# Optimization experiments

Measured on AMD Instinct MI355X. Metric: run time of the kernel, lower is better.

Reference implementation:

```python
import jax, jax.numpy as jnp
import numpy as np

B, T, M, C, H = 32, 128, 1290, 512, 8
NUM_BLOCKS = 4
MLP_LAYERS = 2
TOPK = 8


def _ln(x, g, b):
    mu = jnp.mean(x, -1, keepdims=True)
    var = jnp.mean((x - mu) ** 2, -1, keepdims=True)
    return (x - mu) / jnp.sqrt(var + 1e-5) * g + b


def setup_inputs() -> dict:
    key = jax.random.key(0)
    ks = jax.random.split(key, 12)

    def w(k, shape, s=0.02):
        return jax.random.normal(k, shape, jnp.float32) * s

    return {
        "ipts": jax.random.normal(ks[0], (B, T, C), jnp.float32),
        "memory": jax.random.normal(ks[1], (B, M, C), jnp.float32),
        "Wq": w(ks[2], (C, C)), "bq": jnp.zeros(C, jnp.float32),
        "Wk": w(ks[3], (C, C)), "bk": jnp.zeros(C, jnp.float32),
        "Wv": w(ks[4], (C, C)), "bv": jnp.zeros(C, jnp.float32),
        "Wm": w(ks[5], (C, C)), "bm": jnp.zeros(C, jnp.float32),  # shared attention_mlp layer
        "g1": jnp.ones(C, jnp.float32), "b1": jnp.zeros(C, jnp.float32),
        "g2": jnp.ones(C, jnp.float32), "b2": jnp.zeros(C, jnp.float32),
        "Wp": w(ks[6], (C, C)), "bp": jnp.zeros(C, jnp.float32),
        "rep_w": jax.random.normal(ks[7], (C,), jnp.float32),
        "Wig": w(ks[8], (C, 2 * C)), "big": jnp.zeros(2 * C, jnp.float32),
        "Wmg": w(ks[9], (C, 2 * C)), "bmg": jnp.zeros(2 * C, jnp.float32),
        "forget_bias": jnp.float32(1.0),
        "input_bias": jnp.float32(0.0),
    }


def reference(ipts, memory, Wq, bq, Wk, bk, Wv, bv, Wm, bm, g1, b1, g2, b2,
              Wp, bp, rep_w, Wig, big, Wmg, bmg, forget_bias, input_bias):
    Dh = C // H
    scale = 1.0 / np.sqrt(Dh)

    def heads(x):  # [B,L,C] -> [B,H,L,Dh]
        return x.reshape(x.shape[0], x.shape[1], H, Dh).transpose(0, 2, 1, 3)

    def mha(inp, mem, use_topk):
        # query from mem, key/value from inp (matches multi_head_attention(ipts, memory))
        q, k, v = heads(mem @ Wq + bq), heads(inp @ Wk + bk), heads(inp @ Wv + bv)
        att = jax.nn.softmax(jnp.einsum('bhqd,bhkd->bhqk', q, k) * scale, axis=-1)
        if use_topk:
            _, idx = jax.lax.top_k(att, TOPK)  # [B,H,Q,TOPK]
            mask = jnp.zeros_like(att)
            for i in range(TOPK):  # small fixed loop; avoids [.,.,.,K,L] blowup
                mask = mask + jax.nn.one_hot(idx[..., i], att.shape[-1], dtype=att.dtype)
            att = att * mask
        o = jnp.einsum('bhqk,bhkd->bhqd', att, v)
        return o.transpose(0, 2, 1, 3).reshape(o.shape[0], o.shape[2], C)

    inp = ipts @ Wp + bp  # input_projector, [B,T,C]
    mem = memory
    for _ in range(NUM_BLOCKS):
        mem = _ln(mem + mha(inp, mem, True), g1, b1)
        h = mem
        for _ in range(MLP_LAYERS):  # shared weights (ModuleList([lin]*L))
            h = jax.nn.relu(h @ Wm + bm)
        mem = _ln(mem + h, g2, b2)

    # gates (gate_style='unit')
    gi = jnp.mean(jax.nn.relu(rep_w * inp), axis=1) @ Wig + big  # [B,2C]
    gm = jnp.tanh(memory) @ Wmg + bmg                            # [B,M,2C]
    gates = gm + gi[:, None, :]
    ig = jax.nn.sigmoid(gates[..., :C] + input_bias)
    fg = jax.nn.sigmoid(gates[..., C:] + forget_bias)
    next_memory = ig * jnp.tanh(mem) + fg * memory

    # hx: query from inp, key/value from next_memory, no topk
    hx = mha(next_memory, inp, False)  # [B,T,C]
    return (next_memory, hx)
```

## Files before the change

kernel.cpp:

```cpp
#include <hip/hip_runtime.h>
#include <stdint.h>

typedef uint16_t u16;
typedef uint32_t u32;

#define DEVI __device__ __forceinline__

DEVI float b2f(u16 u) { return __uint_as_float(((u32)u) << 16); }
DEVI float blo(u32 u) { return __uint_as_float(u << 16); }
DEVI float bhi(u32 u) { return __uint_as_float(u & 0xffff0000u); }
DEVI u16 f2b(float f) {
  u32 x = __float_as_uint(f);
  return (u16)((x + 0x7fffu + ((x >> 16) & 1u)) >> 16);
}
DEVI u32 pack2(float a, float b) { return (u32)f2b(a) | ((u32)f2b(b) << 16); }
DEVI float sigm(float x) { return 1.f / (1.f + __expf(-x)); }
DEVI float ftanh(float x) { return 1.f - 2.f / (1.f + __expf(2.f * x)); }

typedef __bf16 bf16x8 __attribute__((ext_vector_type(8)));
typedef float f32x4 __attribute__((ext_vector_type(4)));

#define MFMA16(a, b, c) __builtin_amdgcn_mfma_f32_16x16x32_bf16(a, b, c, 0, 0, 0)

DEVI void gll16(const void* g, void* l) {
  __builtin_amdgcn_global_load_lds((const __attribute__((address_space(1))) void*)g,
                                   (__attribute__((address_space(3))) void*)l, 16, 0, 0);
}

DEVI u32 fmono(float s) {
  u32 x = __float_as_uint(s);
  return x ^ (((u32)((int)x >> 31)) | 0x80000000u);
}

DEVI void ced(u32& a, u32& b) {
  u32 hi = max(a, b), lo = min(a, b);
  a = hi; b = lo;
}
DEVI void sort8_desc(u32* v) {
  ced(v[0], v[1]); ced(v[2], v[3]); ced(v[4], v[5]); ced(v[6], v[7]);
  ced(v[0], v[2]); ced(v[1], v[3]); ced(v[4], v[6]); ced(v[5], v[7]);
  ced(v[1], v[2]); ced(v[5], v[6]);
  ced(v[0], v[4]); ced(v[1], v[5]); ced(v[2], v[6]); ced(v[3], v[7]);
  ced(v[2], v[4]); ced(v[3], v[5]);
  ced(v[1], v[2]); ced(v[3], v[4]); ced(v[5], v[6]);
}
DEVI void bitonic8_desc(u32* v) {
  ced(v[0], v[4]); ced(v[1], v[5]); ced(v[2], v[6]); ced(v[3], v[7]);
  ced(v[0], v[2]); ced(v[1], v[3]); ced(v[4], v[6]); ced(v[5], v[7]);
  ced(v[0], v[1]); ced(v[2], v[3]); ced(v[4], v[5]); ced(v[6], v[7]);
}
DEVI void merge_top8(u32* a, const u32* b) {
#pragma unroll
  for (int j = 0; j < 8; ++j) a[j] = max(a[j], b[7 - j]);
  bitonic8_desc(a);
}

__global__ void detect_kernel(const u16* __restrict__ x, int* __restrict__ flag) {
  if (threadIdx.x == 0 && blockIdx.x == 0) {
    int f = 0;
    for (int i = 0; i < 64; ++i) {
      u16 u = x[2 * i];
      int e = (u >> 7) & 0xFF;
      if (e > 131) f = 1;
    }
    *flag = f;
  }
}

struct CvtArgs {
  const void* src[23];
  int aoff[23];
  int n[23];
  int total;
};

__global__ __launch_bounds__(256) void convert_fused(CvtArgs a, u16* __restrict__ arena,
                                                     const int* __restrict__ flag) {
  int e4 = (blockIdx.x * 256 + threadIdx.x) * 4;
  if (e4 >= a.total) return;
  const char* sp = (const char*)a.src[0];
  int rel = e4, cnt = a.n[0];
#pragma unroll
  for (int j = 1; j < 23; ++j)
    if (e4 >= a.aoff[j]) { sp = (const char*)a.src[j]; rel = e4 - a.aoff[j]; cnt = a.n[j]; }
  const bool f32 = (*flag != 0);
  if (rel + 3 < cnt) {
    if (f32) {
      float4 v = *(const float4*)(sp + (size_t)rel * 4);
      uint2 o;
      o.x = pack2(v.x, v.y);
      o.y = pack2(v.z, v.w);
      *(uint2*)(arena + e4) = o;
    } else {
      *(uint2*)(arena + e4) = *(const uint2*)(sp + (size_t)rel * 2);
    }
  } else {
#pragma unroll
    for (int k = 0; k < 4; ++k) {
      u16 o = 0;
      if (rel + k < cnt)
        o = f32 ? f2b(((const float*)sp)[rel + k]) : ((const u16*)sp)[rel + k];
      arena[e4 + k] = o;
    }
  }
}

__global__ void biascat_kernel(const u16* __restrict__ bq, const u16* __restrict__ bk,
                               const u16* __restrict__ bv, u16* __restrict__ bqkv,
                               u16* __restrict__ bkv) {
  int t = threadIdx.x;
  bqkv[t] = bq[t];
  bqkv[512 + t] = bk[t];
  bqkv[1024 + t] = bv[t];
  bkv[t] = bk[t];
  bkv[512 + t] = bv[t];
}

template <int ACT>
__global__ __launch_bounds__(256, 4) void gemm_bt(
    const u16* __restrict__ A, const u16* __restrict__ Bt,
    const u16* __restrict__ bias, u16* __restrict__ Co, int Mtot, int Ntot, int nby) {
  __shared__ __align__(16) u16 smem[128 * 136];
  u16* const aB0 = smem;
  u16* const aB1 = smem + 4096;
  u16* const bB0 = smem + 8192;
  u16* const bB1 = smem + 12288;
  const int tid = threadIdx.x;
  const int lane = tid & 63;
  const int w = tid >> 6;
  const int quad = lane >> 4;
  const int l15 = lane & 15;

  const int nwg = gridDim.x;
  const int orig = blockIdx.x;
  const int xcd = orig & 7, sq = orig >> 3;
  const int qd = nwg >> 3, rm = nwg & 7;
  const int wg = (xcd < rm ? xcd * (qd + 1) : rm * (qd + 1) + (xcd - rm) * qd) + sq;
  const int m0 = (wg / nby) * 128;
  const int n0 = (wg % nby) * 128;

  const int wm = (w & 1) << 6;
  const int wn = (w >> 1) << 6;

  f32x4 acc[4][4] = {};

  const u16* ga[2];
  const u16* gb[2];
#pragma unroll
  for (int q = 0; q < 2; ++q) {
    int j = q * 256 + tid;
    int r = j >> 2, s = j & 3;
    int c = (s ^ ((r >> 1) & 3)) * 8;
    int ra = m0 + r;
    if (ra >= Mtot) ra = Mtot - 1;
    ga[q] = A + (size_t)ra * 512 + c;
    gb[q] = Bt + (size_t)(n0 + r) * 512 + c;
  }

  auto stage = [&](int p, int ko) {
    u16* ab = p ? aB1 : aB0;
    u16* bb = p ? bB1 : bB0;
#pragma unroll
    for (int q = 0; q < 2; ++q) {
      int j = q * 256 + tid;
      gll16(ga[q] + ko * 32, ab + j * 8);
      gll16(gb[q] + ko * 32, bb + j * 8);
    }
  };

  stage(0, 0);
  __syncthreads();
  int cur = 0;
  for (int ko = 0; ko < 16; ++ko) {
    if (ko < 15) stage(cur ^ 1, ko + 1);
    u16* ab = cur ? aB1 : aB0;
    u16* bb = cur ? bB1 : bB0;
    bf16x8 af[4], bfr[4];
#pragma unroll
    for (int i = 0; i < 4; ++i) {
      int r = wm + i * 16 + l15;
      af[i] = *(const bf16x8*)(ab + (((r << 2) | (quad ^ ((r >> 1) & 3)))) * 8);
      int rn = wn + i * 16 + l15;
      bfr[i] = *(const bf16x8*)(bb + (((rn << 2) | (quad ^ ((rn >> 1) & 3)))) * 8);
    }
#pragma unroll
    for (int i = 0; i < 4; ++i)
#pragma unroll
      for (int jn = 0; jn < 4; ++jn)
        acc[i][jn] = MFMA16(af[i], bfr[jn], acc[i][jn]);
    __syncthreads();
    cur ^= 1;
  }

  u16* st = smem;
  const int cl = l15;
  const int rg = quad;
#pragma unroll
  for (int jn = 0; jn < 4; ++jn) {
    int coll = wn + jn * 16 + cl;
    float bv = b2f(bias[n0 + coll]);
#pragma unroll
    for (int i = 0; i < 4; ++i) {
      int rowb = wm + i * 16 + rg * 4;
#pragma unroll
      for (int rr = 0; rr < 4; ++rr) {
        float vv = acc[i][jn][rr] + bv;
        if (ACT) vv = fmaxf(vv, 0.f);
        st[(rowb + rr) * 136 + coll] = f2b(vv);
      }
    }
  }
  __syncthreads();
#pragma unroll
  for (int t = 0; t < 8; ++t) {
    int idx = (t * 256 + tid) * 8;
    int r = idx >> 7;
    int c = idx & 127;
    int row = m0 + r;
    if (row < Mtot) {
      uint4 v = *(const uint4*)(st + r * 136 + c);
      *(uint4*)(Co + (size_t)row * Ntot + n0 + c) = v;
    }
  }
}

__global__ __launch_bounds__(256, 4) void gemm_gates(
    const u16* __restrict__ A, const u16* __restrict__ WmgTp,
    const u16* __restrict__ bmg, const u16* __restrict__ gi,
    const u16* __restrict__ memfin, const u16* __restrict__ mem_in,
    const u16* __restrict__ ibp, const u16* __restrict__ fbp,
    u16* __restrict__ nmbf, void* __restrict__ outp, const int* __restrict__ flag,
    int Mtot) {
  __shared__ __align__(16) u16 smem[128 * 136];
  u16* const aB0 = smem;
  u16* const aB1 = smem + 4096;
  u16* const bB0 = smem + 8192;
  u16* const bB1 = smem + 12288;
  const int tid = threadIdx.x;
  const int lane = tid & 63;
  const int w = tid >> 6;
  const int quad = lane >> 4;
  const int l15 = lane & 15;

  const int nwg = gridDim.x;
  const int orig = blockIdx.x;
  const int xcd = orig & 7, sq = orig >> 3;
  const int qd = nwg >> 3, rm = nwg & 7;
  const int wg = (xcd < rm ? xcd * (qd + 1) : rm * (qd + 1) + (xcd - rm) * qd) + sq;
  const int m0 = (wg >> 3) * 128;
  const int n0h = (wg & 7) * 64;

  const int wm = (w & 1) << 6;
  const int wn = (w >> 1) << 6;

  f32x4 acc[4][4] = {};

  const u16* ga[2];
  const u16* gb[2];
#pragma unroll
  for (int q = 0; q < 2; ++q) {
    int j = q * 256 + tid;
    int r = j >> 2, s = j & 3;
    int c = (s ^ ((r >> 1) & 3)) * 8;
    int ra = m0 + r;
    if (ra >= Mtot) ra = Mtot - 1;
    ga[q] = A + (size_t)ra * 512 + c;
    int br = (r < 64) ? (n0h + r) : (512 + n0h + r - 64);
    gb[q] = WmgTp + (size_t)br * 512 + c;
  }

  auto stage = [&](int p, int ko) {
    u16* ab = p ? aB1 : aB0;
    u16* bb = p ? bB1 : bB0;
#pragma unroll
    for (int q = 0; q < 2; ++q) {
      int j = q * 256 + tid;
      gll16(ga[q] + ko * 32, ab + j * 8);
      gll16(gb[q] + ko * 32, bb + j * 8);
    }
  };

  stage(0, 0);
  __syncthreads();
  int cur = 0;
  for (int ko = 0; ko < 16; ++ko) {
    if (ko < 15) stage(cur ^ 1, ko + 1);
    u16* ab = cur ? aB1 : aB0;
    u16* bb = cur ? bB1 : bB0;
    bf16x8 af[4], bfr[4];
#pragma unroll
    for (int i = 0; i < 4; ++i) {
      int r = wm + i * 16 + l15;
      af[i] = *(const bf16x8*)(ab + (((r << 2) | (quad ^ ((r >> 1) & 3)))) * 8);
      int rn = wn + i * 16 + l15;
      bfr[i] = *(const bf16x8*)(bb + (((rn << 2) | (quad ^ ((rn >> 1) & 3)))) * 8);
    }
#pragma unroll
    for (int i = 0; i < 4; ++i)
#pragma unroll
      for (int jn = 0; jn < 4; ++jn)
        acc[i][jn] = MFMA16(af[i], bfr[jn], acc[i][jn]);
    __syncthreads();
    cur ^= 1;
  }

  u16* st = smem;
#pragma unroll
  for (int jn = 0; jn < 4; ++jn) {
    int coll = wn + jn * 16 + l15;
    int bcol = (coll < 64) ? (n0h + coll) : (512 + n0h + coll - 64);
    float bv = b2f(bmg[bcol]);
#pragma unroll
    for (int i = 0; i < 4; ++i) {
      int rowb = wm + i * 16 + quad * 4;
#pragma unroll
      for (int rr = 0; rr < 4; ++rr)
        st[(rowb + rr) * 136 + coll] = f2b(acc[i][jn][rr] + bv);
    }
  }
  __syncthreads();

  const float ib = b2f(ibp[0]);
  const float fb = b2f(fbp[0]);
  const bool of32 = (*flag != 0);
#pragma unroll
  for (int t = 0; t < 4; ++t) {
    int chunk = t * 256 + tid;
    int rl = chunk >> 3;
    int c8 = (chunk & 7) * 8;
    int row = m0 + rl;
    if (row >= Mtot) continue;
    int b = row / 1290;
    size_t gidx = (size_t)row * 512 + n0h + c8;
    uint4 uig = *(const uint4*)(st + rl * 136 + c8);
    uint4 ufg = *(const uint4*)(st + rl * 136 + 64 + c8);
    uint4 ugi = *(const uint4*)(gi + b * 1024 + n0h + c8);
    uint4 ugf = *(const uint4*)(gi + b * 1024 + 512 + n0h + c8);
    uint4 umf = *(const uint4*)(memfin + gidx);
    uint4 umi = *(const uint4*)(mem_in + gidx);
    const u32* pig = (const u32*)&uig;
    const u32* pfg = (const u32*)&ufg;
    const u32* pgi = (const u32*)&ugi;
    const u32* pgf = (const u32*)&ugf;
    const u32* pmf = (const u32*)&umf;
    const u32* pmi = (const u32*)&umi;
    float v[8];
#pragma unroll
    for (int k = 0; k < 4; ++k) {
      float ig0 = sigm(blo(pig[k]) + blo(pgi[k]) + ib);
      float ig1 = sigm(bhi(pig[k]) + bhi(pgi[k]) + ib);
      float fg0 = sigm(blo(pfg[k]) + blo(pgf[k]) + fb);
      float fg1 = sigm(bhi(pfg[k]) + bhi(pgf[k]) + fb);
      v[2 * k] = ig0 * ftanh(blo(pmf[k])) + fg0 * blo(pmi[k]);
      v[2 * k + 1] = ig1 * ftanh(bhi(pmf[k])) + fg1 * bhi(pmi[k]);
    }
    uint4 o;
    u32* po = (u32*)&o;
#pragma unroll
    for (int k = 0; k < 4; ++k) po[k] = pack2(v[2 * k], v[2 * k + 1]);
    *(uint4*)(nmbf + gidx) = o;
    if (of32) {
      float4 f0, f1;
      f0.x = v[0]; f0.y = v[1]; f0.z = v[2]; f0.w = v[3];
      f1.x = v[4]; f1.y = v[5]; f1.z = v[6]; f1.w = v[7];
      *(float4*)((float*)outp + gidx) = f0;
      *(float4*)((float*)outp + gidx + 4) = f1;
    } else {
      *(uint4*)((u16*)outp + gidx) = o;
    }
  }
}

__global__ __launch_bounds__(256) void transpose_kernel(const u16* __restrict__ in,
                                                        u16* __restrict__ outb, int K, int N) {
  __shared__ u16 tile[32][33];
  const int tx = threadIdx.x & 31, ty = threadIdx.x >> 5;
  const int bx = blockIdx.x * 32;
  const int by = blockIdx.y * 32;
#pragma unroll
  for (int i = 0; i < 32; i += 8) tile[ty + i][tx] = in[(size_t)(by + ty + i) * N + bx + tx];
  __syncthreads();
#pragma unroll
  for (int i = 0; i < 32; i += 8) outb[(size_t)(bx + ty + i) * K + by + tx] = tile[tx][ty + i];
}

__global__ void tanhmem_kernel(const u16* __restrict__ mi, u16* __restrict__ th, int n8) {
  int i = blockIdx.x * 256 + threadIdx.x;
  if (i >= n8) return;
  uint4 u = ((const uint4*)mi)[i];
  uint4 t;
  t.x = pack2(ftanh(blo(u.x)), ftanh(bhi(u.x)));
  t.y = pack2(ftanh(blo(u.y)), ftanh(bhi(u.y)));
  t.z = pack2(ftanh(blo(u.z)), ftanh(bhi(u.z)));
  t.w = pack2(ftanh(blo(u.w)), ftanh(bhi(u.w)));
  ((uint4*)th)[i] = t;
}

__global__ void redmean_kernel(const u16* __restrict__ inp, const u16* __restrict__ repw,
                               u16* __restrict__ outb) {
  const int b = blockIdx.x;
  const int c = blockIdx.y * 256 + threadIdx.x;
  const float rw = b2f(repw[c]);
  float s = 0.f;
  for (int t = 0; t < 128; ++t)
    s += fmaxf(rw * b2f(inp[(size_t)(b * 128 + t) * 512 + c]), 0.f);
  outb[b * 512 + c] = f2b(s * (1.f / 128.f));
}

__global__ __launch_bounds__(256) void ln_kernel(const u16* __restrict__ src,
                                                 const u16* __restrict__ addb,
                                                 u16* __restrict__ dst,
                                                 const u16* __restrict__ g,
                                                 const u16* __restrict__ bb) {
  const int row = blockIdx.x * 4 + (threadIdx.x >> 6);
  const int lane = threadIdx.x & 63;
  const u16* srow = src + (size_t)row * 512;
  const u16* arow = addb + (size_t)row * 512;
  float x[8];
  float s = 0.f;
#pragma unroll
  for (int i = 0; i < 8; ++i) {
    int c = lane + i * 64;
    x[i] = b2f(srow[c]) + b2f(arow[c]);
    s += x[i];
  }
#pragma unroll
  for (int off = 32; off > 0; off >>= 1) s += __shfl_xor(s, off, 64);
  const float mu = s * (1.f / 512.f);
  float v = 0.f;
#pragma unroll
  for (int i = 0; i < 8; ++i) {
    float d = x[i] - mu;
    v = fmaf(d, d, v);
  }
#pragma unroll
  for (int off = 32; off > 0; off >>= 1) v += __shfl_xor(v, off, 64);
  const float rstd = rsqrtf(v * (1.f / 512.f) + 1e-5f);
  u16* orow = dst + (size_t)row * 512;
#pragma unroll
  for (int i = 0; i < 8; ++i) {
    int c = lane + i * 64;
    orow[c] = f2b(fmaf((x[i] - mu) * rstd, b2f(g[c]), b2f(bb[c])));
  }
}

__global__ __launch_bounds__(256, 3) void attn1_mfma(const u16* __restrict__ q,
                                                     const u16* __restrict__ kb,
                                                     const u16* __restrict__ vb,
                                                     u16* __restrict__ o, int ldkv) {
  __shared__ __align__(16) u16 Pl[128 * 136];
  __shared__ __align__(16) u16 VT[64 * 136];
  __shared__ float lbuf[128];
  u16* Kl = Pl;

  const int tid = threadIdx.x;
  const int lane = tid & 63;
  const int w = tid >> 6;
  const int quad = lane >> 4;
  const int l15 = lane & 15;
  const int qb = blockIdx.x;
  const int bh = blockIdx.y;
  const int b = bh >> 3, h = bh & 7;

#pragma unroll
  for (int qq = 0; qq < 4; ++qq) {
    int j = qq * 256 + tid;
    int r = j >> 3, s = j & 7;
    gll16(kb + (size_t)(b * 128 + r) * ldkv + h * 64 + (s ^ (r & 7)) * 8, Kl + j * 8);
  }
#pragma unroll
  for (int p = 0; p < 4; ++p) {
    int key = (tid & 63) + 64 * (p & 1);
    int dc = w + 4 * (p >> 1);
    uint4 u = *(const uint4*)(vb + (size_t)(b * 128 + key) * ldkv + h * 64 + dc * 8);
    u16 tmp[8];
    *(uint4*)tmp = u;
#pragma unroll
    for (int jj = 0; jj < 8; ++jj) VT[(dc * 8 + jj) * 136 + key] = tmp[jj];
  }

  bf16x8 bq[2][2];
  {
    int ra = min(qb * 128 + w * 32 + l15, 1289);
    int rb_ = min(qb * 128 + w * 32 + 16 + l15, 1289);
    const u16* qa = q + (size_t)(b * 1290 + ra) * 512 + h * 64 + quad * 8;
    const u16* qc = q + (size_t)(b * 1290 + rb_) * 512 + h * 64 + quad * 8;
    bq[0][0] = *(const bf16x8*)(qa);
    bq[0][1] = *(const bf16x8*)(qa + 32);
    bq[1][0] = *(const bf16x8*)(qc);
    bq[1][1] = *(const bf16x8*)(qc + 32);
  }
  __syncthreads();

  f32x4 sa[2][8] = {};
#pragma unroll
  for (int ks = 0; ks < 2; ++ks) {
#pragma unroll
    for (int jn = 0; jn < 8; ++jn) {
      int n = jn * 16 + l15;
      int cch = ks * 4 + quad;
      bf16x8 ak = *(const bf16x8*)(Kl + (n * 8 + (cch ^ (n & 7))) * 8);
      sa[0][jn] = MFMA16(ak, bq[0][ks], sa[0][jn]);
      sa[1][jn] = MFMA16(ak, bq[1][ks], sa[1][jn]);
    }
  }
  __syncthreads();

  const u32 ibase = 127u - (u32)(quad * 4);
#pragma unroll
  for (int i = 0; i < 2; ++i) {
    const int qi = w * 32 + i * 16 + l15;
    u32 g[4][8];
#pragma unroll
    for (int jn = 0; jn < 8; ++jn)
#pragma unroll
      for (int rr = 0; rr < 4; ++rr) {
        float s = sa[i][jn][rr] * 0.125f;
        sa[i][jn][rr] = s;
        g[jn >> 1][(jn & 1) * 4 + rr] =
            (fmono(s) & 0xFFFFFF80u) | (ibase - (u32)(jn * 16 + rr));
      }
    sort8_desc(g[0]); sort8_desc(g[1]); sort8_desc(g[2]); sort8_desc(g[3]);
    merge_top8(g[0], g[1]);
    merge_top8(g[2], g[3]);
    merge_top8(g[0], g[2]);
    u32* tv = g[0];
#pragma unroll
    for (int off = 16; off < 64; off <<= 1) {
      u32 pv[8];
#pragma unroll
      for (int j = 0; j < 8; ++j) pv[j] = (u32)__shfl_xor((int)tv[7 - j], off, 64);
#pragma unroll
      for (int j = 0; j < 8; ++j) tv[j] = max(tv[j], pv[j]);
      bitonic8_desc(tv);
    }
    const u32 t8 = tv[7];
    u32 mb = tv[0] & 0xFFFFFF80u;
    u32 xm = (mb & 0x80000000u) ? (mb ^ 0x80000000u) : ~mb;
    const float mx = __uint_as_float(xm);
    float lsum = 0.f;
#pragma unroll
    for (int jn = 0; jn < 8; ++jn) {
      u16 pr[4];
#pragma unroll
      for (int rr = 0; rr < 4; ++rr) {
        float s = sa[i][jn][rr];
        float e = __expf(s - mx);
        lsum += e;
        u32 kk = (fmono(s) & 0xFFFFFF80u) | (ibase - (u32)(jn * 16 + rr));
        pr[rr] = (kk >= t8) ? f2b(e) : (u16)0;
      }
      uint2 st;
      st.x = (u32)pr[0] | ((u32)pr[1] << 16);
      st.y = (u32)pr[2] | ((u32)pr[3] << 16);
      *(uint2*)(Pl + qi * 136 + jn * 16 + quad * 4) = st;
    }
    lsum += __shfl_xor(lsum, 16, 64);
    lsum += __shfl_xor(lsum, 32, 64);
    if (quad == 0) lbuf[qi] = 1.f / lsum;
  }
  __syncthreads();

  f32x4 oa[2][4] = {};
#pragma unroll
  for (int kc = 0; kc < 4; ++kc) {
    bf16x8 ap[2];
#pragma unroll
    for (int i = 0; i < 2; ++i)
      ap[i] = *(const bf16x8*)(Pl + (w * 32 + i * 16 + l15) * 136 + kc * 32 + quad * 8);
#pragma unroll
    for (int jd = 0; jd < 4; ++jd) {
      bf16x8 bv_ = *(const bf16x8*)(VT + (jd * 16 + l15) * 136 + kc * 32 + quad * 8);
      oa[0][jd] = MFMA16(ap[0], bv_, oa[0][jd]);
      oa[1][jd] = MFMA16(ap[1], bv_, oa[1][jd]);
    }
  }

#pragma unroll
  for (int i = 0; i < 2; ++i) {
    int rowl = w * 32 + i * 16 + quad * 4;
#pragma unroll
    for (int rr = 0; rr < 4; ++rr) {
      int qg = qb * 128 + rowl + rr;
      if (qg < 1290) {
        float il = lbuf[rowl + rr];
        u16* orow = o + (size_t)(b * 1290 + qg) * 512 + h * 64;
#pragma unroll
        for (int jd = 0; jd < 4; ++jd) orow[jd * 16 + l15] = f2b(oa[i][jd][rr] * il);
      }
    }
  }
}

__global__ __launch_bounds__(256, 2) void attn2_mfma(const u16* __restrict__ q2,
                                                     const u16* __restrict__ k2,
                                                     const u16* __restrict__ v2,
                                                     float* __restrict__ pacc,
                                                     float* __restrict__ pml,
                                                     int ldq, int ldkv) {
  __shared__ __align__(16) u16 Kl[64 * 64];
  __shared__ __align__(16) u16 VT[64 * 72];
  __shared__ __align__(16) u16 Pl[4 * 32 * 72];
  const int tid = threadIdx.x;
  const int lane = tid & 63;
  const int w = tid >> 6;
  const int quad = lane >> 4;
  const int l15 = lane & 15;
  const int bh = blockIdx.x;
  const int b = bh >> 3, h = bh & 7;
  const int part = blockIdx.y;
  const int kstart = (part * 1290) >> 2;
  const int kend = ((part + 1) * 1290) >> 2;

  bf16x8 aq[2][2];
  {
    int r0 = b * 128 + w * 32 + l15;
    const u16* qa = q2 + (size_t)r0 * ldq + h * 64 + quad * 8;
    aq[0][0] = *(const bf16x8*)(qa);
    aq[0][1] = *(const bf16x8*)(qa + 32);
    aq[1][0] = *(const bf16x8*)(qa + (size_t)16 * ldq);
    aq[1][1] = *(const bf16x8*)(qa + (size_t)16 * ldq + 32);
  }

  f32x4 oa[2][4] = {};
  float m_[2][4], l_[2][4];
#pragma unroll
  for (int i = 0; i < 2; ++i)
#pragma unroll
    for (int r = 0; r < 4; ++r) { m_[i][r] = -1e30f; l_[i][r] = 0.f; }

  const int nk = kend - kstart;
  for (int kt = 0; kt < nk; kt += 64) {
    __syncthreads();
#pragma unroll
    for (int qq = 0; qq < 2; ++qq) {
      int j = qq * 256 + tid;
      int r = j >> 3, s = j & 7;
      int kg = kstart + kt + r;
      if (kg >= kend) kg = kend - 1;
      gll16(k2 + (size_t)(b * 1290 + kg) * ldkv + h * 64 + (s ^ (r & 7)) * 8, Kl + j * 8);
    }
    {
      int r = tid & 63;
      int kg = kstart + kt + r;
      if (kg >= kend) kg = kend - 1;
      const u16* vrow = v2 + (size_t)(b * 1290 + kg) * ldkv + h * 64;
#pragma unroll
      for (int p = 0; p < 2; ++p) {
        int dc = (tid >> 6) + p * 4;
        uint4 u = *(const uint4*)(vrow + dc * 8);
        u16 tmp[8];
        *(uint4*)tmp = u;
#pragma unroll
        for (int jj = 0; jj < 8; ++jj) VT[(dc * 8 + jj) * 72 + r] = tmp[jj];
      }
    }
    __syncthreads();

    f32x4 sa[2][4] = {};
#pragma unroll
    for (int ks = 0; ks < 2; ++ks) {
#pragma unroll
      for (int jn = 0; jn < 4; ++jn) {
        int n = jn * 16 + l15;
        int cch = ks * 4 + quad;
        bf16x8 bk = *(const bf16x8*)(Kl + (n * 8 + (cch ^ (n & 7))) * 8);
        sa[0][jn] = MFMA16(aq[0][ks], bk, sa[0][jn]);
        sa[1][jn] = MFMA16(aq[1][ks], bk, sa[1][jn]);
      }
    }

    u16* pw = Pl + w * (32 * 72);
#pragma unroll
    for (int i = 0; i < 2; ++i) {
      float rmax[4] = {-1e30f, -1e30f, -1e30f, -1e30f};
#pragma unroll
      for (int jn = 0; jn < 4; ++jn) {
        int kg = kstart + kt + jn * 16 + l15;
        bool val = kg < kend;
#pragma unroll
        for (int r = 0; r < 4; ++r) {
          float s = sa[i][jn][r] * 0.125f;
          s = val ? s : -1e30f;
          sa[i][jn][r] = s;
          rmax[r] = fmaxf(rmax[r], s);
        }
      }
#pragma unroll
      for (int off = 1; off < 16; off <<= 1)
#pragma unroll
        for (int r = 0; r < 4; ++r) rmax[r] = fmaxf(rmax[r], __shfl_xor(rmax[r], off, 64));
      float alpha[4];
#pragma unroll
      for (int r = 0; r < 4; ++r) {
        float mn = fmaxf(m_[i][r], rmax[r]);
        alpha[r] = __expf(m_[i][r] - mn);
        m_[i][r] = mn;
      }
      float lsum[4] = {0.f, 0.f, 0.f, 0.f};
#pragma unroll
      for (int jn = 0; jn < 4; ++jn)
#pragma unroll
        for (int r = 0; r < 4; ++r) {
          float p = __expf(sa[i][jn][r] - m_[i][r]);
          sa[i][jn][r] = p;
          lsum[r] += p;
        }
#pragma unroll
      for (int off = 1; off < 16; off <<= 1)
#pragma unroll
        for (int r = 0; r < 4; ++r) lsum[r] += __shfl_xor(lsum[r], off, 64);
#pragma unroll
      for (int r = 0; r < 4; ++r) l_[i][r] = l_[i][r] * alpha[r] + lsum[r];
#pragma unroll
      for (int jd = 0; jd < 4; ++jd)
#pragma unroll
        for (int r = 0; r < 4; ++r) oa[i][jd][r] *= alpha[r];
#pragma unroll
      for (int jn = 0; jn < 4; ++jn) {
        int col = jn * 16 + l15;
#pragma unroll
        for (int r = 0; r < 4; ++r)
          pw[(i * 16 + quad * 4 + r) * 72 + col] = f2b(sa[i][jn][r]);
      }
    }

#pragma unroll
    for (int ks = 0; ks < 2; ++ks) {
      bf16x8 ap[2];
#pragma unroll
      for (int i = 0; i < 2; ++i)
        ap[i] = *(const bf16x8*)(pw + (i * 16 + l15) * 72 + ks * 32 + quad * 8);
#pragma unroll
      for (int jd = 0; jd < 4; ++jd) {
        bf16x8 bv_ = *(const bf16x8*)(VT + (jd * 16 + l15) * 72 + ks * 32 + quad * 8);
        oa[0][jd] = MFMA16(ap[0], bv_, oa[0][jd]);
        oa[1][jd] = MFMA16(ap[1], bv_, oa[1][jd]);
      }
    }
  }

  float* pa = pacc + (size_t)(part * 256 + bh) * 128 * 64;
#pragma unroll
  for (int i = 0; i < 2; ++i) {
    int row = w * 32 + i * 16 + quad * 4;
#pragma unroll
    for (int r = 0; r < 4; ++r)
#pragma unroll
      for (int jd = 0; jd < 4; ++jd)
        pa[(size_t)(row + r) * 64 + jd * 16 + l15] = oa[i][jd][r];
    if (l15 == 0) {
#pragma unroll
      for (int r = 0; r < 4; ++r) {
        size_t pi = (size_t)(part * 256 + bh) * 128 + row + r;
        pml[pi * 2 + 0] = m_[i][r];
        pml[pi * 2 + 1] = l_[i][r];
      }
    }
  }
}

__global__ __launch_bounds__(64) void attn2_merge(const float* __restrict__ pacc,
                                                  const float* __restrict__ pml,
                                                  void* __restrict__ outp,
                                                  const int* __restrict__ flag) {
  const int qi = blockIdx.x;
  const int bh = qi >> 7, t = qi & 127;
  const int b = bh >> 3, h = bh & 7;
  const int lane = threadIdx.x;
  float mv[4], lv[4];
  float m0 = -1e30f;
#pragma unroll
  for (int i = 0; i < 4; ++i) {
    size_t pi = (size_t)(i * 256 + bh) * 128 + t;
    mv[i] = pml[pi * 2];
    lv[i] = pml[pi * 2 + 1];
    m0 = fmaxf(m0, mv[i]);
  }
  float L = 0.f, accd = 0.f;
#pragma unroll
  for (int i = 0; i < 4; ++i) {
    size_t pi = (size_t)(i * 256 + bh) * 128 + t;
    float e = __expf(mv[i] - m0);
    L += lv[i] * e;
    accd += pacc[pi * 64 + lane] * e;
  }
  float v = accd / L;
  size_t off = (size_t)41280 * 512 + ((size_t)(b * 128 + t) * 512 + h * 64 + lane);
  if (*flag) ((float*)outp)[off] = v; else ((u16*)outp)[off] = f2b(v);
}

extern "C" void kernel_launch(void* const* d_in, const int* in_sizes, int n_in,
                              void* d_out, int out_size, void* d_ws, size_t ws_size,
                              hipStream_t stream) {
  (void)out_size; (void)ws_size;
  char* ws = (char*)d_ws;
  size_t off = 0;
  auto alloc = [&](size_t bytes) {
    char* p = ws + off;
    off += (bytes + 255) & ~(size_t)255;
    return (void*)p;
  };

  int* flag = (int*)alloc(256);

  size_t aoffs[32];
  size_t total = 0;
  for (int i = 0; i < n_in; ++i) {
    aoffs[i] = total;
    total += ((size_t)in_sizes[i] + 127) & ~(size_t)127;
  }
  u16* arena = (u16*)alloc(total * 2);

  const u16* c_ipts = arena + aoffs[0];
  const u16* c_mem  = arena + aoffs[1];
  const u16* c_Wq = arena + aoffs[2];  const u16* c_bq = arena + aoffs[3];
  const u16* c_Wk = arena + aoffs[4];  const u16* c_bk = arena + aoffs[5];
  const u16* c_Wv = arena + aoffs[6];  const u16* c_bv = arena + aoffs[7];
  const u16* c_Wm = arena + aoffs[8];  const u16* c_bm = arena + aoffs[9];
  const u16* c_g1 = arena + aoffs[10]; const u16* c_b1 = arena + aoffs[11];
  const u16* c_g2 = arena + aoffs[12]; const u16* c_b2 = arena + aoffs[13];
  const u16* c_Wp = arena + aoffs[14]; const u16* c_bp = arena + aoffs[15];
  const u16* c_repw = arena + aoffs[16];
  const u16* c_Wig = arena + aoffs[17]; const u16* c_big = arena + aoffs[18];
  const u16* c_Wmg = arena + aoffs[19]; const u16* c_bmg = arena + aoffs[20];
  const u16* c_fb = arena + aoffs[21];
  const u16* c_ib = arena + aoffs[22];

  u16* WqkvT = (u16*)alloc((size_t)1536 * 512 * 2);
  u16* WmT = (u16*)alloc(512 * 512 * 2);
  u16* WpT = (u16*)alloc(512 * 512 * 2);
  u16* WigT = (u16*)alloc(512 * 1024 * 2);
  u16* WmgT = (u16*)alloc(512 * 1024 * 2);
  u16* bqkv = (u16*)alloc(1536 * 2);
  u16* bkv = (u16*)alloc(1024 * 2);
  u16* inp = (u16*)alloc((size_t)4096 * 512 * 2);
  u16* qkvbuf = (u16*)alloc((size_t)4096 * 1536 * 2);
  u16* rmean = (u16*)alloc(32 * 512 * 2);
  u16* gi = (u16*)alloc(32 * 1024 * 2);
  u16* membf = (u16*)alloc((size_t)41280 * 512 * 2);
  u16* qbuf = (u16*)alloc((size_t)41280 * 512 * 2);
  u16* obuf = (u16*)alloc((size_t)41280 * 512 * 2);
  u16* gmbuf = (u16*)alloc((size_t)41280 * 512 * 2);
  u16* nmbf = (u16*)alloc((size_t)41280 * 512 * 2);
  (void)gmbuf;
  u16* kvbuf = obuf;
  float* pacc = (float*)(void*)qbuf;
  float* pml = (float*)((char*)(void*)qbuf + (size_t)4 * 32768 * 64 * 4);

  detect_kernel<<<1, 64, 0, stream>>>((const u16*)d_in[0], flag);
  {
    CvtArgs ca;
    for (int i = 0; i < 23; ++i) {
      int ii = (i < n_in) ? i : (n_in - 1);
      ca.src[i] = d_in[ii];
      ca.aoff[i] = (int)aoffs[ii];
      ca.n[i] = in_sizes[ii];
    }
    ca.total = (int)total;
    convert_fused<<<(unsigned)((total / 4 + 255) / 256), 256, 0, stream>>>(ca, arena, flag);
  }
  biascat_kernel<<<1, 512, 0, stream>>>(c_bq, c_bk, c_bv, bqkv, bkv);

  transpose_kernel<<<dim3(16, 16), 256, 0, stream>>>(c_Wq, WqkvT, 512, 512);
  transpose_kernel<<<dim3(16, 16), 256, 0, stream>>>(c_Wk, WqkvT + (size_t)512 * 512, 512, 512);
  transpose_kernel<<<dim3(16, 16), 256, 0, stream>>>(c_Wv, WqkvT + (size_t)1024 * 512, 512, 512);
  transpose_kernel<<<dim3(16, 16), 256, 0, stream>>>(c_Wm, WmT, 512, 512);
  transpose_kernel<<<dim3(16, 16), 256, 0, stream>>>(c_Wp, WpT, 512, 512);
  transpose_kernel<<<dim3(32, 16), 256, 0, stream>>>(c_Wig, WigT, 512, 1024);
  transpose_kernel<<<dim3(32, 16), 256, 0, stream>>>(c_Wmg, WmgT, 512, 1024);

  gemm_bt<0><<<dim3(32 * 4), 256, 0, stream>>>(c_ipts, WpT, c_bp, inp, 4096, 512, 4);
  gemm_bt<0><<<dim3(32 * 12), 256, 0, stream>>>(inp, WqkvT, bqkv, qkvbuf, 4096, 1536, 12);

  redmean_kernel<<<dim3(32, 2), 256, 0, stream>>>(inp, c_repw, rmean);
  gemm_bt<0><<<dim3(1 * 8), 256, 0, stream>>>(rmean, WigT, c_big, gi, 32, 1024, 8);

  const u16* memsrc = c_mem;
  for (int it = 0; it < 4; ++it) {
    gemm_bt<0><<<dim3(323 * 4), 256, 0, stream>>>(memsrc, WqkvT, c_bq, qbuf, 41280, 512, 4);
    attn1_mfma<<<dim3(11, 256), 256, 0, stream>>>(qbuf, qkvbuf + 512, qkvbuf + 1024, obuf, 1536);
    ln_kernel<<<dim3(10320), 256, 0, stream>>>(memsrc, obuf, membf, c_g1, c_b1);
    gemm_bt<1><<<dim3(323 * 4), 256, 0, stream>>>(membf, WmT, c_bm, qbuf, 41280, 512, 4);
    gemm_bt<1><<<dim3(323 * 4), 256, 0, stream>>>(qbuf, WmT, c_bm, obuf, 41280, 512, 4);
    ln_kernel<<<dim3(10320), 256, 0, stream>>>(membf, obuf, membf, c_g2, c_b2);
    memsrc = membf;
  }

  tanhmem_kernel<<<dim3(2641920 / 256), 256, 0, stream>>>(c_mem, qbuf, 2641920);
  gemm_gates<<<dim3(323 * 8), 256, 0, stream>>>(qbuf, WmgT, c_bmg, gi, membf, c_mem,
                                                c_ib, c_fb, nmbf, d_out, flag, 41280);

  gemm_bt<0><<<dim3(323 * 8), 256, 0, stream>>>(nmbf, WqkvT + (size_t)512 * 512, bkv,
                                                kvbuf, 41280, 1024, 8);
  attn2_mfma<<<dim3(256, 4), 256, 0, stream>>>(qkvbuf, kvbuf, kvbuf + 512, pacc, pml,
                                               1536, 1024);
  attn2_merge<<<dim3(32768), 64, 0, stream>>>(pacc, pml, d_out, flag);
}
```

Baseline: 1.188 ms.

## Fuse two shared-weight MLP layers and second layernorm into one kernel

Replaces the two MLP GEMM launches and the following layernorm with a single kernel that keeps a 64-row tile of the first layer's activations in LDS, runs the second GEMM from LDS, and applies residual plus layernorm in registers before writing back in place. This removes the global-memory round trips of two full-size intermediate activations and two launches per block iteration. In exchange it uses large LDS per block (lower occupancy), loads weight fragments directly from global/L2 without LDS staging, and has fewer blocks than the original tiled GEMMs.

```diff
diff --git a/kernel.cpp b/kernel.cpp
--- a/kernel.cpp
+++ b/kernel.cpp
@@ -221,6 +221,150 @@
       uint4 v = *(const uint4*)(st + r * 136 + c);
       *(uint4*)(Co + (size_t)row * Ntot + n0 + c) = v;
     }
+  }
+}
+
+__global__ __launch_bounds__(256, 2) void gemm_mlp_ln(
+    u16* __restrict__ mem, const u16* __restrict__ WmT, const u16* __restrict__ bm,
+    const u16* __restrict__ g2, const u16* __restrict__ b2) {
+  __shared__ __align__(16) u16 h1[64 * 512];
+  __shared__ __align__(16) u16 ast[2][64 * 32];
+  __shared__ float red[4][64][2];
+  const int tid = threadIdx.x;
+  const int lane = tid & 63;
+  const int w = tid >> 6;
+  const int quad = lane >> 4;
+  const int l15 = lane & 15;
+  const int m0 = blockIdx.x * 64;
+  const int nw = w * 128;
+
+  const int sr = tid >> 2, ss = tid & 3;
+  const u16* ga = mem + (size_t)(m0 + sr) * 512 + ((ss ^ ((sr >> 1) & 3)) * 8);
+
+  f32x4 acc[4][8] = {};
+
+  gll16(ga, &ast[0][0] + tid * 8);
+  __syncthreads();
+  for (int ko = 0; ko < 16; ++ko) {
+    if (ko < 15) gll16(ga + (ko + 1) * 32, &ast[(ko + 1) & 1][0] + tid * 8);
+    const u16* ab = &ast[ko & 1][0];
+    bf16x8 af[4];
+#pragma unroll
+    for (int i = 0; i < 4; ++i) {
+      int r = i * 16 + l15;
+      af[i] = *(const bf16x8*)(ab + (((r << 2) | (quad ^ ((r >> 1) & 3)))) * 8);
+    }
+#pragma unroll
+    for (int j = 0; j < 8; ++j) {
+      int col = nw + j * 16 + l15;
+      bf16x8 bfr = *(const bf16x8*)(WmT + (size_t)col * 512 + ko * 32 + quad * 8);
+#pragma unroll
+      for (int i = 0; i < 4; ++i) acc[i][j] = MFMA16(af[i], bfr, acc[i][j]);
+    }
+    __syncthreads();
+  }
+
+#pragma unroll
+  for (int j = 0; j < 8; ++j) {
+    int col = nw + j * 16 + l15;
+    float bv = b2f(bm[col]);
+    int chunk = col >> 3, cin = col & 7;
+#pragma unroll
+    for (int i = 0; i < 4; ++i)
+#pragma unroll
+      for (int rr = 0; rr < 4; ++rr) {
+        int row = i * 16 + quad * 4 + rr;
+        h1[row * 512 + ((chunk ^ (row & 7)) << 3) + cin] =
+            f2b(fmaxf(acc[i][j][rr] + bv, 0.f));
+      }
+  }
+  __syncthreads();
+
+#pragma unroll
+  for (int i = 0; i < 4; ++i)
+#pragma unroll
+    for (int j = 0; j < 8; ++j) acc[i][j] = (f32x4){0.f, 0.f, 0.f, 0.f};
+  for (int ko = 0; ko < 16; ++ko) {
+    bf16x8 af[4];
+#pragma unroll
+    for (int i = 0; i < 4; ++i) {
+      int r = i * 16 + l15;
+      af[i] = *(const bf16x8*)(h1 + r * 512 + ((((ko << 2) + quad) ^ (r & 7)) << 3));
+    }
+#pragma unroll
+    for (int j = 0; j < 8; ++j) {
+      int col = nw + j * 16 + l15;
+      bf16x8 bfr = *(const bf16x8*)(WmT + (size_t)col * 512 + ko * 32 + quad * 8);
+#pragma unroll
+      for (int i = 0; i < 4; ++i) acc[i][j] = MFMA16(af[i], bfr, acc[i][j]);
+    }
+  }
+
+  float ps[4][4], pq[4][4];
+#pragma unroll
+  for (int i = 0; i < 4; ++i)
+#pragma unroll
+    for (int rr = 0; rr < 4; ++rr) { ps[i][rr] = 0.f; pq[i][rr] = 0.f; }
+#pragma unroll
+  for (int j = 0; j < 8; ++j) {
+    int col = nw + j * 16 + l15;
+    float bv = b2f(bm[col]);
+#pragma unroll
+    for (int i = 0; i < 4; ++i)
+#pragma unroll
+      for (int rr = 0; rr < 4; ++rr) {
+        int row = i * 16 + quad * 4 + rr;
+        float h2 = fmaxf(acc[i][j][rr] + bv, 0.f);
+        float x = b2f(f2b(h2)) + b2f(mem[(size_t)(m0 + row) * 512 + col]);
+        acc[i][j][rr] = x;
+        ps[i][rr] += x;
+        pq[i][rr] = fmaf(x, x, pq[i][rr]);
+      }
+  }
+#pragma unroll
+  for (int off = 1; off < 16; off <<= 1)
+#pragma unroll
+    for (int i = 0; i < 4; ++i)
+#pragma unroll
+      for (int rr = 0; rr < 4; ++rr) {
+        ps[i][rr] += __shfl_xor(ps[i][rr], off, 64);
+        pq[i][rr] += __shfl_xor(pq[i][rr], off, 64);
+      }
+  if (l15 == 0) {
+#pragma unroll
+    for (int i = 0; i < 4; ++i)
+#pragma unroll
+      for (int rr = 0; rr < 4; ++rr) {
+        int row = i * 16 + quad * 4 + rr;
+        red[w][row][0] = ps[i][rr];
+        red[w][row][1] = pq[i][rr];
+      }
+  }
+  __syncthreads();
+
+#pragma unroll
+  for (int i = 0; i < 4; ++i)
+#pragma unroll
+    for (int rr = 0; rr < 4; ++rr) {
+      int row = i * 16 + quad * 4 + rr;
+      float s = red[0][row][0] + red[1][row][0] + red[2][row][0] + red[3][row][0];
+      float q = red[0][row][1] + red[1][row][1] + red[2][row][1] + red[3][row][1];
+      float mu = s * (1.f / 512.f);
+      float var = fmaxf(q * (1.f / 512.f) - mu * mu, 0.f);
+      float rstd = rsqrtf(var + 1e-5f);
+#pragma unroll
+      for (int j = 0; j < 8; ++j) {
+        int col = nw + j * 16 + l15;
+        h1[row * 512 + col] =
+            f2b(fmaf((acc[i][j][rr] - mu) * rstd, b2f(g2[col]), b2f(b2[col])));
+      }
+    }
+  __syncthreads();
+#pragma unroll
+  for (int t = 0; t < 16; ++t) {
+    int idx = (t * 256 + tid) * 8;
+    int row = idx >> 9, col = idx & 511;
+    *(uint4*)(mem + (size_t)(m0 + row) * 512 + col) = *(const uint4*)(h1 + row * 512 + col);
   }
 }
 
@@ -881,9 +1025,7 @@
     gemm_bt<0><<<dim3(323 * 4), 256, 0, stream>>>(memsrc, WqkvT, c_bq, qbuf, 41280, 512, 4);
     attn1_mfma<<<dim3(11, 256), 256, 0, stream>>>(qbuf, qkvbuf + 512, qkvbuf + 1024, obuf, 1536);
     ln_kernel<<<dim3(10320), 256, 0, stream>>>(memsrc, obuf, membf, c_g1, c_b1);
-    gemm_bt<1><<<dim3(323 * 4), 256, 0, stream>>>(membf, WmT, c_bm, qbuf, 41280, 512, 4);
-    gemm_bt<1><<<dim3(323 * 4), 256, 0, stream>>>(qbuf, WmT, c_bm, obuf, 41280, 512, 4);
-    ln_kernel<<<dim3(10320), 256, 0, stream>>>(membf, obuf, membf, c_g2, c_b2);
+    gemm_mlp_ln<<<dim3(645), 256, 0, stream>>>(membf, WmT, c_bm, c_g2, c_b2);
     memsrc = membf;
   }
 
```

Result: slower. 1.765 ms (+48.5%).
